# Kernel tuning notes

Measured on AMD Instinct MI355X. Metric: run time of the kernel, lower is better.

The kernel has to match this reference:

```python
import jax, jax.numpy as jnp
import numpy as np

N_NODES = 100000
N_EDGES = 1600000
IN_DIM = 128
HEADS = 4
OUT_DIM = 32
NEG_SLOPE = 0.2  # DGL GATConv default


def setup_inputs() -> dict:
    key = jax.random.key(0)
    ks = jax.random.split(key, 7)
    x = jax.random.normal(ks[0], (N_NODES, IN_DIM), dtype=jnp.float32)
    edge_src = jax.random.randint(ks[1], (N_EDGES,), 0, N_NODES, dtype=jnp.int32)
    edge_dst = jax.random.randint(ks[2], (N_EDGES,), 0, N_NODES, dtype=jnp.int32)
    # Xavier-ish init for the projection / attention params
    fc_w = jax.random.normal(ks[3], (IN_DIM, HEADS * OUT_DIM), dtype=jnp.float32) / np.sqrt(IN_DIM)
    attn_l = jax.random.normal(ks[4], (HEADS, OUT_DIM), dtype=jnp.float32) / np.sqrt(OUT_DIM)
    attn_r = jax.random.normal(ks[5], (HEADS, OUT_DIM), dtype=jnp.float32) / np.sqrt(OUT_DIM)
    bias = jnp.zeros((HEADS * OUT_DIM,), dtype=jnp.float32)
    return {"x": x, "edge_src": edge_src, "edge_dst": edge_dst,
            "fc_w": fc_w, "attn_l": attn_l, "attn_r": attn_r, "bias": bias}


def reference(x, edge_src, edge_dst, fc_w, attn_l, attn_r, bias):
    N = x.shape[0]
    H, D = attn_l.shape
    # Linear projection, per-head features [N, H, D]
    feat = (x @ fc_w).reshape(N, H, D)
    # Per-node attention logits [N, H]
    el = jnp.einsum('nhd,hd->nh', feat, attn_l)
    er = jnp.einsum('nhd,hd->nh', feat, attn_r)
    # Per-edge scores e_{u->v} = leaky_relu(el[u] + er[v])  [E, H]
    e = jax.nn.leaky_relu(el[edge_src] + er[edge_dst], NEG_SLOPE)
    # Edge softmax segmented over destination node (stable via segment max)
    m = jax.ops.segment_max(e, edge_dst, num_segments=N)  # [N, H]
    m = jnp.where(jnp.isfinite(m), m, jnp.float32(0))      # zero in-degree nodes
    ex = jnp.exp(e - jax.lax.stop_gradient(m)[edge_dst])
    s = jax.ops.segment_sum(ex, edge_dst, num_segments=N)  # [N, H]
    alpha = ex / jnp.maximum(s[edge_dst], jnp.float32(1e-16))  # [E, H]
    # Weighted neighbor aggregation  out[v] = sum_u alpha * feat[u]
    msg = alpha[:, :, None] * feat[edge_src]               # [E, H, D]
    out = jax.ops.segment_sum(msg, edge_dst, num_segments=N)  # [N, H, D]
    out = out + bias.reshape(1, H, D)
    # Head mean as in the wrapper's .mean(dim=1)
    return out.mean(axis=1)  # [N, D]
```

## Files before the change

kernel.cpp:

```cpp
#include <hip/hip_runtime.h>

#define IN_DIM 128
#define HEADS 4
#define OUT_DIM 32
#define NEG 0.2f

#define NPB 256
#define NB_MAX 400
#define EPB 8192

typedef unsigned int uint;
typedef unsigned short ushort_t;
typedef short short8 __attribute__((ext_vector_type(8)));
typedef float f32x4 __attribute__((ext_vector_type(4)));
typedef uint u32x4 __attribute__((ext_vector_type(4)));

__device__ __forceinline__ uint bf16r(float f) {
    uint u = __float_as_uint(f);
    return (u + 0x7fffu + ((u >> 16) & 1u)) >> 16;
}

__global__ __launch_bounds__(256) void wt_prep_kernel(
    const float* __restrict__ fc_w, const float* __restrict__ attn_l,
    const float* __restrict__ attn_r,
    ushort_t* __restrict__ wt, ushort_t* __restrict__ wt2)
{
    int t = blockIdx.x * 256 + threadIdx.x;
    int n = t >> 7, k = t & 127;
    wt[t] = (ushort_t)bf16r(fc_w[k * 128 + n]);
    if (t < 2048) {
        int col = t >> 7;
        int kk  = t & 127;
        float ssum = 0.f;
        if (col < 8) {
            int h = col & 3;
            const float* av = (col < 4) ? attn_l : attn_r;
            #pragma unroll 8
            for (int d = 0; d < 32; ++d)
                ssum += fc_w[kk * 128 + h * 32 + d] * av[h * 32 + d];
        }
        wt2[col * 128 + kk] = (ushort_t)bf16r(ssum);
    }
}

__global__ __launch_bounds__(256) void proj_hist_kernel(
    const float* __restrict__ x, const ushort_t* __restrict__ wt,
    const ushort_t* __restrict__ wt2,
    ushort_t* __restrict__ feat16, float* __restrict__ el, float* __restrict__ er,
    int N,
    const int* __restrict__ edst, int* __restrict__ bucketCount, int E, int NB,
    int nblkE)
{
    __shared__ int hbuf[NB_MAX];

    if ((int)blockIdx.x < nblkE) {
        for (int t = threadIdx.x; t < NB_MAX; t += 256) hbuf[t] = 0;
        __syncthreads();
        const int base = blockIdx.x * EPB;
        #pragma unroll
        for (int rep = 0; rep < EPB / 1024; ++rep) {
            int i = base + (rep * 256 + threadIdx.x) * 4;
            if (i + 3 < E) {
                int4 d = *(const int4*)(edst + i);
                atomicAdd(&hbuf[d.x >> 8], 1);
                atomicAdd(&hbuf[d.y >> 8], 1);
                atomicAdd(&hbuf[d.z >> 8], 1);
                atomicAdd(&hbuf[d.w >> 8], 1);
            } else {
                for (int k = 0; k < 4; ++k)
                    if (i + k < E) atomicAdd(&hbuf[edst[i + k] >> 8], 1);
            }
        }
        __syncthreads();
        for (int t = threadIdx.x; t < NB; t += 256)
            if (hbuf[t]) atomicAdd(&bucketCount[t], hbuf[t]);
        return;
    }

    const int pblk = (int)blockIdx.x - nblkE;
    const int lane = threadIdx.x & 63;
    const int w    = threadIdx.x >> 6;
    const int rowbase = pblk * 64 + w * 16;
    const int c = lane & 15;
    const int g = lane >> 4;

    f32x4 acc[8];
    #pragma unroll
    for (int nt = 0; nt < 8; ++nt) acc[nt] = (f32x4){0.f, 0.f, 0.f, 0.f};
    f32x4 acc8v = (f32x4){0.f, 0.f, 0.f, 0.f};

    const int arow  = rowbase + c;
    const int arowc = (arow < N) ? arow : (N - 1);
    const float* xrow = x + (size_t)arowc * 128 + g * 8;

    #pragma unroll
    for (int kk = 0; kk < 4; ++kk) {
        const float* xp = xrow + kk * 32;
        float4 f0 = *(const float4*)xp;
        float4 f1 = *(const float4*)(xp + 4);
        u32x4 au;
        au.x = bf16r(f0.x) | (bf16r(f0.y) << 16);
        au.y = bf16r(f0.z) | (bf16r(f0.w) << 16);
        au.z = bf16r(f1.x) | (bf16r(f1.y) << 16);
        au.w = bf16r(f1.z) | (bf16r(f1.w) << 16);
        short8 afrag = __builtin_bit_cast(short8, au);
        #pragma unroll
        for (int nt = 0; nt < 8; ++nt) {
            const ushort_t* wp = wt + ((nt * 16 + c) * 128 + kk * 32 + g * 8);
            u32x4 bu = *(const u32x4*)wp;
            short8 bfrag = __builtin_bit_cast(short8, bu);
            acc[nt] = __builtin_amdgcn_mfma_f32_16x16x32_bf16(afrag, bfrag, acc[nt], 0, 0, 0);
        }
        {
            const ushort_t* wp2 = wt2 + (c * 128 + kk * 32 + g * 8);
            u32x4 bu2 = *(const u32x4*)wp2;
            short8 bfrag2 = __builtin_bit_cast(short8, bu2);
            acc8v = __builtin_amdgcn_mfma_f32_16x16x32_bf16(afrag, bfrag2, acc8v, 0, 0, 0);
        }
    }

    #pragma unroll
    for (int r = 0; r < 4; ++r) {
        const int node = rowbase + g * 4 + r;
        if (node < N) {
            ushort_t* fp = feat16 + (size_t)node * 128 + c;
            #pragma unroll
            for (int nt = 0; nt < 8; ++nt) {
                fp[nt * 16] = (ushort_t)bf16r(acc[nt][r]);
            }
            if (c < 4)       el[node * 4 + c]       = acc8v[r];
            else if (c < 8)  er[node * 4 + (c - 4)] = acc8v[r];
        }
    }
}

__global__ __launch_bounds__(512) void bucket_scan_kernel(
    const int* __restrict__ bucketCount, int* __restrict__ bucketStart,
    int* __restrict__ bucketCursor, int* __restrict__ row_start, int NB, int N)
{
    __shared__ int p[512];
    const int t = threadIdx.x;
    int v = (t < NB) ? bucketCount[t] : 0;
    p[t] = v;
    __syncthreads();
    for (int off = 1; off < 512; off <<= 1) {
        int u = (t >= off) ? p[t - off] : 0;
        __syncthreads();
        p[t] += u;
        __syncthreads();
    }
    if (t < NB) {
        bucketStart[t]  = p[t] - v;
        bucketCursor[t] = p[t] - v;
    }
    if (t == NB - 1) {
        bucketStart[NB] = p[t];
        row_start[N]    = p[t];
    }
}

__global__ __launch_bounds__(256) void bin_kernel(
    const int* __restrict__ esrc, const int* __restrict__ edst,
    int* __restrict__ bucketCursor, uint* __restrict__ binned, int E, int NB)
{
    __shared__ int dstS[EPB];
    __shared__ int hist[NB_MAX];
    __shared__ int cur[NB_MAX];
    const int t = threadIdx.x;
    for (int k = t; k < NB_MAX; k += 256) hist[k] = 0;
    __syncthreads();

    const int base = blockIdx.x * EPB;
    #pragma unroll
    for (int rep = 0; rep < EPB / 1024; ++rep) {
        int idx4 = (rep * 256 + t) * 4;
        int i = base + idx4;
        if (i + 3 < E) {
            int4 d = *(const int4*)(edst + i);
            dstS[idx4]     = d.x; atomicAdd(&hist[d.x >> 8], 1);
            dstS[idx4 + 1] = d.y; atomicAdd(&hist[d.y >> 8], 1);
            dstS[idx4 + 2] = d.z; atomicAdd(&hist[d.z >> 8], 1);
            dstS[idx4 + 3] = d.w; atomicAdd(&hist[d.w >> 8], 1);
        } else {
            for (int k = 0; k < 4; ++k)
                if (i + k < E) {
                    int dv = edst[i + k];
                    dstS[idx4 + k] = dv;
                    atomicAdd(&hist[dv >> 8], 1);
                }
        }
    }
    __syncthreads();
    for (int k = t; k < NB; k += 256) {
        int hh = hist[k];
        cur[k] = hh ? atomicAdd(&bucketCursor[k], hh) : 0;
    }
    __syncthreads();
    const int nloc = min(EPB, E - base);
    for (int rep = 0; rep < EPB / 256; ++rep) {
        int idx = rep * 256 + t;
        if (idx < nloc) {
            int dv = dstS[idx];
            int pos = atomicAdd(&cur[dv >> 8], 1);
            int src = esrc[base + idx];
            binned[pos] = (uint)src | ((uint)(dv & 255) << 24);
        }
    }
}

__global__ __launch_bounds__(256) void fine_csr_kernel(
    const uint* __restrict__ binned, const int* __restrict__ bucketStart,
    int* __restrict__ row_start, int* __restrict__ csr, int N)
{
    __shared__ int hist[256], sc[256], cur[256];
    const int b = blockIdx.x;
    const int t = threadIdx.x;
    const int s = bucketStart[b];
    const int e = bucketStart[b + 1];

    hist[t] = 0;
    __syncthreads();
    for (int i = s + t; i < e; i += 256)
        atomicAdd(&hist[binned[i] >> 24], 1);
    __syncthreads();
    sc[t] = hist[t];
    __syncthreads();
    for (int off = 1; off < 256; off <<= 1) {
        int u = (t >= off) ? sc[t - off] : 0;
        __syncthreads();
        sc[t] += u;
        __syncthreads();
    }
    const int excl = s + sc[t] - hist[t];
    const int gn = b * NPB + t;
    if (gn < N) row_start[gn] = excl;
    cur[t] = excl;
    __syncthreads();
    for (int i = s + t; i < e; i += 256) {
        uint v = binned[i];
        int pos = atomicAdd(&cur[v >> 24], 1);
        csr[pos] = (int)(v & 0xFFFFFFu);
    }
}

__global__ __launch_bounds__(256) void aggregate_kernel(
    const u32x4* __restrict__ feat4, const float* __restrict__ el,
    const float* __restrict__ er, const int* __restrict__ row_start,
    const int* __restrict__ csr, const float* __restrict__ bias,
    float* __restrict__ out, int N)
{
    int node = blockIdx.x * 4 + (threadIdx.x >> 6);
    node = __builtin_amdgcn_readfirstlane(node);
    if (node >= N) return;
    const int lane = threadIdx.x & 63;
    const int g  = lane >> 4;
    const int ll = lane & 15;
    const int h  = ll >> 2;

    const int start = row_start[node];
    const int end   = row_start[node + 1];
    const float er_v = er[node * 4 + h];

    float rA0=0.f,rA1=0.f,rA2=0.f,rA3=0.f,rA4=0.f,rA5=0.f,rA6=0.f,rA7=0.f;
    float rB0=0.f,rB1=0.f,rB2=0.f,rB3=0.f,rB4=0.f,rB5=0.f,rB6=0.f,rB7=0.f;
    float sA = 0.f, sB = 0.f;
    const int last = end - 1;

    for (int i0 = start; i0 < end; i0 += 8) {
        const int iA = i0 + g;
        const int iB = i0 + 4 + g;
        const bool vA = iA < end;
        const bool vB = iB < end;
        const int uA = csr[vA ? iA : last];
        const int uB = csr[vB ? iB : last];
        float eA = el[uA * 4 + h];
        float eB = el[uB * 4 + h];
        u32x4 pA = feat4[(size_t)uA * 16 + ll];
        u32x4 pB = feat4[(size_t)uB * 16 + ll];

        eA += er_v; eA = fmaxf(eA, NEG * eA);
        float xA = vA ? __expf(eA) : 0.f;
        eB += er_v; eB = fmaxf(eB, NEG * eB);
        float xB = vB ? __expf(eB) : 0.f;
        sA += xA; sB += xB;

        rA0 = fmaf(xA, __uint_as_float(pA.x << 16),         rA0);
        rA1 = fmaf(xA, __uint_as_float(pA.x & 0xffff0000u), rA1);
        rA2 = fmaf(xA, __uint_as_float(pA.y << 16),         rA2);
        rA3 = fmaf(xA, __uint_as_float(pA.y & 0xffff0000u), rA3);
        rA4 = fmaf(xA, __uint_as_float(pA.z << 16),         rA4);
        rA5 = fmaf(xA, __uint_as_float(pA.z & 0xffff0000u), rA5);
        rA6 = fmaf(xA, __uint_as_float(pA.w << 16),         rA6);
        rA7 = fmaf(xA, __uint_as_float(pA.w & 0xffff0000u), rA7);
        rB0 = fmaf(xB, __uint_as_float(pB.x << 16),         rB0);
        rB1 = fmaf(xB, __uint_as_float(pB.x & 0xffff0000u), rB1);
        rB2 = fmaf(xB, __uint_as_float(pB.y << 16),         rB2);
        rB3 = fmaf(xB, __uint_as_float(pB.y & 0xffff0000u), rB3);
        rB4 = fmaf(xB, __uint_as_float(pB.z << 16),         rB4);
        rB5 = fmaf(xB, __uint_as_float(pB.z & 0xffff0000u), rB5);
        rB6 = fmaf(xB, __uint_as_float(pB.w << 16),         rB6);
        rB7 = fmaf(xB, __uint_as_float(pB.w & 0xffff0000u), rB7);
    }

    float r0 = rA0 + rB0, r1 = rA1 + rB1, r2 = rA2 + rB2, r3 = rA3 + rB3;
    float r4 = rA4 + rB4, r5 = rA5 + rB5, r6 = rA6 + rB6, r7 = rA7 + rB7;
    float s = sA + sB;

    s  += __shfl_xor(s, 16);  s  += __shfl_xor(s, 32);
    r0 += __shfl_xor(r0, 16); r0 += __shfl_xor(r0, 32);
    r1 += __shfl_xor(r1, 16); r1 += __shfl_xor(r1, 32);
    r2 += __shfl_xor(r2, 16); r2 += __shfl_xor(r2, 32);
    r3 += __shfl_xor(r3, 16); r3 += __shfl_xor(r3, 32);
    r4 += __shfl_xor(r4, 16); r4 += __shfl_xor(r4, 32);
    r5 += __shfl_xor(r5, 16); r5 += __shfl_xor(r5, 32);
    r6 += __shfl_xor(r6, 16); r6 += __shfl_xor(r6, 32);
    r7 += __shfl_xor(r7, 16); r7 += __shfl_xor(r7, 32);

    s = fmaxf(s, 1e-16f);
    r0 /= s; r1 /= s; r2 /= s; r3 /= s;
    r4 /= s; r5 /= s; r6 /= s; r7 /= s;

    r0 += __shfl_xor(r0, 4); r0 += __shfl_xor(r0, 8);
    r1 += __shfl_xor(r1, 4); r1 += __shfl_xor(r1, 8);
    r2 += __shfl_xor(r2, 4); r2 += __shfl_xor(r2, 8);
    r3 += __shfl_xor(r3, 4); r3 += __shfl_xor(r3, 8);
    r4 += __shfl_xor(r4, 4); r4 += __shfl_xor(r4, 8);
    r5 += __shfl_xor(r5, 4); r5 += __shfl_xor(r5, 8);
    r6 += __shfl_xor(r6, 4); r6 += __shfl_xor(r6, 8);
    r7 += __shfl_xor(r7, 4); r7 += __shfl_xor(r7, 8);

    if (lane < 4) {
        const int m0 = lane * 8;
        float4 o0, o1;
        o0.x = 0.25f * (r0 + bias[m0]   + bias[32+m0]   + bias[64+m0]   + bias[96+m0]);
        o0.y = 0.25f * (r1 + bias[m0+1] + bias[33+m0]   + bias[65+m0]   + bias[97+m0]);
        o0.z = 0.25f * (r2 + bias[m0+2] + bias[34+m0]   + bias[66+m0]   + bias[98+m0]);
        o0.w = 0.25f * (r3 + bias[m0+3] + bias[35+m0]   + bias[67+m0]   + bias[99+m0]);
        o1.x = 0.25f * (r4 + bias[m0+4] + bias[36+m0]   + bias[68+m0]   + bias[100+m0]);
        o1.y = 0.25f * (r5 + bias[m0+5] + bias[37+m0]   + bias[69+m0]   + bias[101+m0]);
        o1.z = 0.25f * (r6 + bias[m0+6] + bias[38+m0]   + bias[70+m0]   + bias[102+m0]);
        o1.w = 0.25f * (r7 + bias[m0+7] + bias[39+m0]   + bias[71+m0]   + bias[103+m0]);
        float* op = out + (size_t)node * 32 + m0;
        *(float4*)op       = o0;
        *(float4*)(op + 4) = o1;
    }
}

extern "C" void kernel_launch(void* const* d_in, const int* in_sizes, int n_in,
                              void* d_out, int out_size, void* d_ws, size_t ws_size,
                              hipStream_t stream)
{
    const float* x      = (const float*)d_in[0];
    const int*   esrc   = (const int*)  d_in[1];
    const int*   edst   = (const int*)  d_in[2];
    const float* fc_w   = (const float*)d_in[3];
    const float* attn_l = (const float*)d_in[4];
    const float* attn_r = (const float*)d_in[5];
    const float* bias   = (const float*)d_in[6];
    float* out = (float*)d_out;

    const int N = in_sizes[0] / IN_DIM;
    const int E = in_sizes[1];
    const int NB = (N + NPB - 1) / NPB;

    size_t o = 0;
    char* base = (char*)d_ws;
    auto alloc = [&](size_t bytes) -> void* {
        void* p = base + o;
        o += (bytes + 255) & ~(size_t)255;
        return p;
    };
    ushort_t* feat16   = (ushort_t*)alloc((size_t)N * 128 * sizeof(ushort_t));
    float* el          = (float*)alloc((size_t)N * 4 * sizeof(float));
    float* er          = (float*)alloc((size_t)N * 4 * sizeof(float));
    int*   row_start   = (int*)  alloc(((size_t)N + 1) * sizeof(int));
    int*   csr         = (int*)  alloc((size_t)E * sizeof(int));
    uint*  binned      = (uint*) alloc((size_t)E * sizeof(uint));
    int*   bucketCount = (int*)  alloc(NB_MAX * sizeof(int));
    int*   bucketStart = (int*)  alloc((NB_MAX + 1) * sizeof(int));
    int*   bucketCursor= (int*)  alloc(NB_MAX * sizeof(int));
    ushort_t* wt       = (ushort_t*)alloc((size_t)128 * 128 * sizeof(ushort_t));
    ushort_t* wt2      = (ushort_t*)alloc((size_t)16 * 128 * sizeof(ushort_t));
    (void)ws_size;

    const int nblkE = (E + EPB - 1) / EPB;
    const int nblkP = (N + 63) / 64;

    hipMemsetAsync(bucketCount, 0, NB_MAX * sizeof(int), stream);

    wt_prep_kernel<<<64, 256, 0, stream>>>(fc_w, attn_l, attn_r, wt, wt2);
    proj_hist_kernel<<<nblkE + nblkP, 256, 0, stream>>>(
        x, wt, wt2, feat16, el, er, N,
        edst, bucketCount, E, NB, nblkE);
    bucket_scan_kernel<<<1, 512, 0, stream>>>(bucketCount, bucketStart,
                                              bucketCursor, row_start, NB, N);
    bin_kernel<<<nblkE, 256, 0, stream>>>(esrc, edst, bucketCursor, binned, E, NB);
    fine_csr_kernel<<<NB, 256, 0, stream>>>(binned, bucketStart, row_start, csr, N);
    aggregate_kernel<<<(N + 3) / 4, 256, 0, stream>>>((const u32x4*)feat16, el, er,
                                                      row_start, csr, bias, out, N);
}
```

Baseline: 164.5 us.

## Split projection across bin and fine-CSR kernels to fill underused launches

Merges the weight-prep kernel with the destination histogram and removes one launch. The node projection is split in half: one half runs as extra blocks in the bin kernel and the other as extra blocks in the fine CSR kernel, so it overlaps with those small, latency-bound kernels. The bin kernel no longer stages destinations in a 32KB shared buffer; it re-reads edst from global memory, which should raise occupancy at the cost of an extra global read. The aggregate kernel also replaces eight divisions with one reciprocal and eight multiplies.

```diff
diff --git a/kernel.cpp b/kernel.cpp
--- a/kernel.cpp
+++ b/kernel.cpp
@@ -20,64 +20,12 @@
     return (u + 0x7fffu + ((u >> 16) & 1u)) >> 16;
 }
 
-__global__ __launch_bounds__(256) void wt_prep_kernel(
-    const float* __restrict__ fc_w, const float* __restrict__ attn_l,
-    const float* __restrict__ attn_r,
-    ushort_t* __restrict__ wt, ushort_t* __restrict__ wt2)
-{
-    int t = blockIdx.x * 256 + threadIdx.x;
-    int n = t >> 7, k = t & 127;
-    wt[t] = (ushort_t)bf16r(fc_w[k * 128 + n]);
-    if (t < 2048) {
-        int col = t >> 7;
-        int kk  = t & 127;
-        float ssum = 0.f;
-        if (col < 8) {
-            int h = col & 3;
-            const float* av = (col < 4) ? attn_l : attn_r;
-            #pragma unroll 8
-            for (int d = 0; d < 32; ++d)
-                ssum += fc_w[kk * 128 + h * 32 + d] * av[h * 32 + d];
-        }
-        wt2[col * 128 + kk] = (ushort_t)bf16r(ssum);
-    }
-}
-
-__global__ __launch_bounds__(256) void proj_hist_kernel(
-    const float* __restrict__ x, const ushort_t* __restrict__ wt,
+__device__ __forceinline__ void proj_body(
+    int pblk, const float* __restrict__ x, const ushort_t* __restrict__ wt,
     const ushort_t* __restrict__ wt2,
     ushort_t* __restrict__ feat16, float* __restrict__ el, float* __restrict__ er,
-    int N,
-    const int* __restrict__ edst, int* __restrict__ bucketCount, int E, int NB,
-    int nblkE)
-{
-    __shared__ int hbuf[NB_MAX];
-
-    if ((int)blockIdx.x < nblkE) {
-        for (int t = threadIdx.x; t < NB_MAX; t += 256) hbuf[t] = 0;
-        __syncthreads();
-        const int base = blockIdx.x * EPB;
-        #pragma unroll
-        for (int rep = 0; rep < EPB / 1024; ++rep) {
-            int i = base + (rep * 256 + threadIdx.x) * 4;
-            if (i + 3 < E) {
-                int4 d = *(const int4*)(edst + i);
-                atomicAdd(&hbuf[d.x >> 8], 1);
-                atomicAdd(&hbuf[d.y >> 8], 1);
-                atomicAdd(&hbuf[d.z >> 8], 1);
-                atomicAdd(&hbuf[d.w >> 8], 1);
-            } else {
-                for (int k = 0; k < 4; ++k)
-                    if (i + k < E) atomicAdd(&hbuf[edst[i + k] >> 8], 1);
-            }
-        }
-        __syncthreads();
-        for (int t = threadIdx.x; t < NB; t += 256)
-            if (hbuf[t]) atomicAdd(&bucketCount[t], hbuf[t]);
-        return;
-    }
-
-    const int pblk = (int)blockIdx.x - nblkE;
+    int N)
+{
     const int lane = threadIdx.x & 63;
     const int w    = threadIdx.x >> 6;
     const int rowbase = pblk * 64 + w * 16;
@@ -134,6 +82,57 @@
     }
 }
 
+__global__ __launch_bounds__(256) void prep_hist_kernel(
+    const float* __restrict__ fc_w, const float* __restrict__ attn_l,
+    const float* __restrict__ attn_r,
+    ushort_t* __restrict__ wt, ushort_t* __restrict__ wt2,
+    const int* __restrict__ edst, int* __restrict__ bucketCount, int E, int NB)
+{
+    __shared__ int hbuf[NB_MAX];
+
+    if (blockIdx.x < 64) {
+        int t = blockIdx.x * 256 + threadIdx.x;
+        int n = t >> 7, k = t & 127;
+        wt[t] = (ushort_t)bf16r(fc_w[k * 128 + n]);
+        if (t < 2048) {
+            int col = t >> 7;
+            int kk  = t & 127;
+            float ssum = 0.f;
+            if (col < 8) {
+                int h = col & 3;
+                const float* av = (col < 4) ? attn_l : attn_r;
+                #pragma unroll 8
+                for (int d = 0; d < 32; ++d)
+                    ssum += fc_w[kk * 128 + h * 32 + d] * av[h * 32 + d];
+            }
+            wt2[col * 128 + kk] = (ushort_t)bf16r(ssum);
+        }
+        return;
+    }
+
+    const int hblk = (int)blockIdx.x - 64;
+    for (int t = threadIdx.x; t < NB_MAX; t += 256) hbuf[t] = 0;
+    __syncthreads();
+    const int base = hblk * EPB;
+    #pragma unroll
+    for (int rep = 0; rep < EPB / 1024; ++rep) {
+        int i = base + (rep * 256 + threadIdx.x) * 4;
+        if (i + 3 < E) {
+            int4 d = *(const int4*)(edst + i);
+            atomicAdd(&hbuf[d.x >> 8], 1);
+            atomicAdd(&hbuf[d.y >> 8], 1);
+            atomicAdd(&hbuf[d.z >> 8], 1);
+            atomicAdd(&hbuf[d.w >> 8], 1);
+        } else {
+            for (int k = 0; k < 4; ++k)
+                if (i + k < E) atomicAdd(&hbuf[edst[i + k] >> 8], 1);
+        }
+    }
+    __syncthreads();
+    for (int t = threadIdx.x; t < NB; t += 256)
+        if (hbuf[t]) atomicAdd(&bucketCount[t], hbuf[t]);
+}
+
 __global__ __launch_bounds__(512) void bucket_scan_kernel(
     const int* __restrict__ bucketCount, int* __restrict__ bucketStart,
     int* __restrict__ bucketCursor, int* __restrict__ row_start, int NB, int N)
@@ -159,13 +158,23 @@
     }
 }
 
-__global__ __launch_bounds__(256) void bin_kernel(
+__global__ __launch_bounds__(256) void bin_proj_kernel(
     const int* __restrict__ esrc, const int* __restrict__ edst,
-    int* __restrict__ bucketCursor, uint* __restrict__ binned, int E, int NB)
-{
-    __shared__ int dstS[EPB];
+    int* __restrict__ bucketCursor, uint* __restrict__ binned, int E, int NB,
+    int nblkE,
+    const float* __restrict__ x, const ushort_t* __restrict__ wt,
+    const ushort_t* __restrict__ wt2,
+    ushort_t* __restrict__ feat16, float* __restrict__ el, float* __restrict__ er,
+    int N)
+{
     __shared__ int hist[NB_MAX];
     __shared__ int cur[NB_MAX];
+
+    if ((int)blockIdx.x >= nblkE) {
+        proj_body((int)blockIdx.x - nblkE, x, wt, wt2, feat16, el, er, N);
+        return;
+    }
+
     const int t = threadIdx.x;
     for (int k = t; k < NB_MAX; k += 256) hist[k] = 0;
     __syncthreads();
@@ -173,21 +182,16 @@
     const int base = blockIdx.x * EPB;
     #pragma unroll
     for (int rep = 0; rep < EPB / 1024; ++rep) {
-        int idx4 = (rep * 256 + t) * 4;
-        int i = base + idx4;
+        int i = base + (rep * 256 + t) * 4;
         if (i + 3 < E) {
             int4 d = *(const int4*)(edst + i);
-            dstS[idx4]     = d.x; atomicAdd(&hist[d.x >> 8], 1);
-            dstS[idx4 + 1] = d.y; atomicAdd(&hist[d.y >> 8], 1);
-            dstS[idx4 + 2] = d.z; atomicAdd(&hist[d.z >> 8], 1);
-            dstS[idx4 + 3] = d.w; atomicAdd(&hist[d.w >> 8], 1);
+            atomicAdd(&hist[d.x >> 8], 1);
+            atomicAdd(&hist[d.y >> 8], 1);
+            atomicAdd(&hist[d.z >> 8], 1);
+            atomicAdd(&hist[d.w >> 8], 1);
         } else {
             for (int k = 0; k < 4; ++k)
-                if (i + k < E) {
-                    int dv = edst[i + k];
-                    dstS[idx4 + k] = dv;
-                    atomicAdd(&hist[dv >> 8], 1);
-                }
+                if (i + k < E) atomicAdd(&hist[edst[i + k] >> 8], 1);
         }
     }
     __syncthreads();
@@ -200,7 +204,7 @@
     for (int rep = 0; rep < EPB / 256; ++rep) {
         int idx = rep * 256 + t;
         if (idx < nloc) {
-            int dv = dstS[idx];
+            int dv = edst[base + idx];
             int pos = atomicAdd(&cur[dv >> 8], 1);
             int src = esrc[base + idx];
             binned[pos] = (uint)src | ((uint)(dv & 255) << 24);
@@ -208,11 +212,21 @@
     }
 }
 
-__global__ __launch_bounds__(256) void fine_csr_kernel(
+__global__ __launch_bounds__(256) void fine_proj_kernel(
     const uint* __restrict__ binned, const int* __restrict__ bucketStart,
-    int* __restrict__ row_start, int* __restrict__ csr, int N)
+    int* __restrict__ row_start, int* __restrict__ csr, int N, int NBb,
+    int projOffset,
+    const float* __restrict__ x, const ushort_t* __restrict__ wt,
+    const ushort_t* __restrict__ wt2,
+    ushort_t* __restrict__ feat16, float* __restrict__ el, float* __restrict__ er)
 {
     __shared__ int hist[256], sc[256], cur[256];
+
+    if ((int)blockIdx.x >= NBb) {
+        proj_body((int)blockIdx.x - NBb + projOffset, x, wt, wt2, feat16, el, er, N);
+        return;
+    }
+
     const int b = blockIdx.x;
     const int t = threadIdx.x;
     const int s = bucketStart[b];
@@ -317,8 +331,9 @@
     r7 += __shfl_xor(r7, 16); r7 += __shfl_xor(r7, 32);
 
     s = fmaxf(s, 1e-16f);
-    r0 /= s; r1 /= s; r2 /= s; r3 /= s;
-    r4 /= s; r5 /= s; r6 /= s; r7 /= s;
+    float inv = 1.0f / s;
+    r0 *= inv; r1 *= inv; r2 *= inv; r3 *= inv;
+    r4 *= inv; r5 *= inv; r6 *= inv; r7 *= inv;
 
     r0 += __shfl_xor(r0, 4); r0 += __shfl_xor(r0, 8);
     r1 += __shfl_xor(r1, 4); r1 += __shfl_xor(r1, 8);
@@ -385,17 +400,21 @@
 
     const int nblkE = (E + EPB - 1) / EPB;
     const int nblkP = (N + 63) / 64;
+    const int projA = nblkP / 2;
+    const int projB = nblkP - projA;
 
     hipMemsetAsync(bucketCount, 0, NB_MAX * sizeof(int), stream);
 
-    wt_prep_kernel<<<64, 256, 0, stream>>>(fc_w, attn_l, attn_r, wt, wt2);
-    proj_hist_kernel<<<nblkE + nblkP, 256, 0, stream>>>(
-        x, wt, wt2, feat16, el, er, N,
-        edst, bucketCount, E, NB, nblkE);
+    prep_hist_kernel<<<64 + nblkE, 256, 0, stream>>>(
+        fc_w, attn_l, attn_r, wt, wt2, edst, bucketCount, E, NB);
     bucket_scan_kernel<<<1, 512, 0, stream>>>(bucketCount, bucketStart,
                                               bucketCursor, row_start, NB, N);
-    bin_kernel<<<nblkE, 256, 0, stream>>>(esrc, edst, bucketCursor, binned, E, NB);
-    fine_csr_kernel<<<NB, 256, 0, stream>>>(binned, bucketStart, row_start, csr, N);
+    bin_proj_kernel<<<nblkE + projA, 256, 0, stream>>>(
+        esrc, edst, bucketCursor, binned, E, NB, nblkE,
+        x, wt, wt2, feat16, el, er, N);
+    fine_proj_kernel<<<NB + projB, 256, 0, stream>>>(
+        binned, bucketStart, row_start, csr, N, NB, projA,
+        x, wt, wt2, feat16, el, er);
     aggregate_kernel<<<(N + 3) / 4, 256, 0, stream>>>((const u32x4*)feat16, el, er,
                                                       row_start, csr, bias, out, N);
 }
```

Measured after the change: 162.1 us. Within noise of the previous version (-1.4%).
